# Optimization experiments

Hardware: AMD Instinct MI355X
Metric: run time of the kernel (lower is better)

Reference implementation:

```python
import jax, jax.numpy as jnp
import numpy as np

DIM = 256
HEADS = 8
HEAD_DIM = DIM // HEADS
WS = (2, 8, 8)  # window size (t, h, w)
N = WS[0] * WS[1] * WS[2]  # 128 tokens per window
SCALE = HEAD_DIM ** -0.5
MLP_HIDDEN = int(DIM * 2.0)
EPS = 1e-5

# static relative-position index table [N, N]
def _rel_pos_index():
    coords = np.stack(np.meshgrid(np.arange(WS[0]), np.arange(WS[1]), np.arange(WS[2]), indexing='ij'))
    cf = coords.reshape(3, -1)
    rel = cf[:, :, None] - cf[:, None, :]
    rel = rel.transpose(1, 2, 0).copy()
    rel[..., 0] += WS[0] - 1
    rel[..., 1] += WS[1] - 1
    rel[..., 2] += WS[2] - 1
    rel[..., 0] *= (2 * WS[1] - 1) * (2 * WS[2] - 1)
    rel[..., 1] *= (2 * WS[2] - 1)
    return rel.sum(-1)

REL_IDX = jnp.asarray(_rel_pos_index())  # [N, N] int
TABLE_SIZE = (2 * WS[0] - 1) * (2 * WS[1] - 1) * (2 * WS[2] - 1)  # 675


def layernorm(x, g, b):
    m = jnp.mean(x, axis=-1, keepdims=True)
    var = jnp.mean(jnp.square(x - m), axis=-1, keepdims=True)
    return (x - m) * jax.lax.rsqrt(var + EPS) * g + b


def window_partition(x):
    B, T, H, W, C = x.shape
    x = x.reshape(B, T // WS[0], WS[0], H // WS[1], WS[1], W // WS[2], WS[2], C)
    x = x.transpose(0, 1, 3, 5, 2, 4, 6, 7)
    return x.reshape(-1, N, C)


def window_reverse(wins, B, T, H, W):
    C = wins.shape[-1]
    x = wins.reshape(B, T // WS[0], H // WS[1], W // WS[2], WS[0], WS[1], WS[2], C)
    x = x.transpose(0, 1, 4, 2, 5, 3, 6, 7)
    return x.reshape(B, T, H, W, C)


def setup_inputs() -> dict:
    key = jax.random.key(0)
    ks = jax.random.split(key, 20)
    B, T, H, W = 2, 8, 64, 64
    f = lambda k, s, sc=0.02: jax.random.normal(k, s, dtype=jnp.float32) * sc
    return {
        'q': jax.random.normal(ks[0], (B, T, H, W, DIM), dtype=jnp.float32),
        'k': jax.random.normal(ks[1], (B, T, H, W, DIM), dtype=jnp.float32),
        'v': jax.random.normal(ks[2], (B, T, H, W, DIM), dtype=jnp.float32),
        'gq': jnp.ones((DIM,), jnp.float32), 'bq': jnp.zeros((DIM,), jnp.float32),
        'gk': jnp.ones((DIM,), jnp.float32), 'bk': jnp.zeros((DIM,), jnp.float32),
        'gv': jnp.ones((DIM,), jnp.float32), 'bv': jnp.zeros((DIM,), jnp.float32),
        'bias_table': f(ks[3], (TABLE_SIZE, HEADS)),
        'proj_w': f(ks[4], (DIM, DIM)), 'proj_b': jnp.zeros((DIM,), jnp.float32),
        'g2': jnp.ones((DIM,), jnp.float32), 'b2': jnp.zeros((DIM,), jnp.float32),
        'mw1': f(ks[5], (MLP_HIDDEN, DIM)), 'mb1': jnp.zeros((MLP_HIDDEN,), jnp.float32),
        'mw2': f(ks[6], (DIM, MLP_HIDDEN)), 'mb2': jnp.zeros((DIM,), jnp.float32),
    }


def reference(q, k, v, gq, bq, gk, bk, gv, bv, bias_table, proj_w, proj_b, g2, b2, mw1, mb1, mw2, mb2):
    B, T, H, W, C = q.shape
    shortcut = v
    qn = layernorm(q, gq, bq)
    kn = layernorm(k, gk, bk)
    vn = layernorm(v, gv, bv)
    # (dims divisible by window -> no padding needed)
    qw = window_partition(qn)  # [B_, N, C]
    kw = window_partition(kn)
    vw = window_partition(vn)
    B_ = qw.shape[0]
    to_heads = lambda t: t.reshape(B_, N, HEADS, HEAD_DIM).transpose(0, 2, 1, 3)  # [B_, h, N, d]
    qh, kh, vh = to_heads(qw), to_heads(kw), to_heads(vw)
    attn = jnp.einsum('bhnd,bhmd->bhnm', qh * SCALE, kh)
    bias = bias_table[REL_IDX]  # [N, N, heads]
    attn = attn + bias.transpose(2, 0, 1)[None]
    attn = jax.nn.softmax(attn, axis=-1)
    out = jnp.einsum('bhnm,bhmd->bhnd', attn, vh)
    out = out.transpose(0, 2, 1, 3).reshape(B_, N, C)
    out = out @ proj_w.T + proj_b
    x = window_reverse(out, B, T, H, W)
    x = shortcut + x
    h1 = layernorm(x, g2, b2)
    h1 = jax.nn.gelu(h1 @ mw1.T + mb1, approximate=False)
    x = x + (h1 @ mw2.T + mb2)
    return x
```

## Files before the change

kernel.cpp:

```cpp
#include <hip/hip_runtime.h>
#include <math.h>


typedef __attribute__((ext_vector_type(8))) short short8;
typedef __attribute__((ext_vector_type(4))) short shortx4;
typedef __attribute__((ext_vector_type(4))) float floatx4;

#define MFMA16(a, b, c) __builtin_amdgcn_mfma_f32_16x16x32_bf16((a), (b), (c), 0, 0, 0)
#define ATT_SCALE 0.17677669529663689f

__device__ __forceinline__ short f2bf(float f) {
  unsigned u = __float_as_uint(f);
  u += 0x7fffu + ((u >> 16) & 1u);
  return (short)(u >> 16);
}
__device__ __forceinline__ float bf2f(short s) {
  return __uint_as_float(((unsigned)(unsigned short)s) << 16);
}
__device__ __forceinline__ void gl2lds(const short* g, short* l) {
  __builtin_amdgcn_global_load_lds((const __attribute__((address_space(1))) void*)(g),
                                   (__attribute__((address_space(3))) void*)(l), 16, 0, 0);
}

__global__ void cvt_kernel(const float* __restrict__ src, short* __restrict__ dst, int n) {
  int i = blockIdx.x * 256 + threadIdx.x;
  if (i < n) dst[i] = f2bf(src[i]);
}

__global__ void biasprep_kernel(const float* __restrict__ table, short* __restrict__ biasPb) {
  int idx = blockIdx.x * 256 + threadIdx.x;
  int h = idx >> 14;
  int n = (idx >> 7) & 127;
  int lr = (idx >> 3) & 15;
  int c = idx & 7;
  int m = 16 * c + lr;
  int t1 = n >> 6, h1 = (n >> 3) & 7, w1 = n & 7;
  int t2 = m >> 6, h2 = (m >> 3) & 7, w2 = m & 7;
  int ridx = (t1 - t2 + 1) * 225 + (h1 - h2 + 7) * 15 + (w1 - w2 + 7);
  biasPb[idx] = f2bf(table[ridx * 8 + h]);
}

__global__ __launch_bounds__(256) void ln_qkv_kernel(
    const float* __restrict__ q, const float* __restrict__ k, const float* __restrict__ v,
    const float* __restrict__ gq, const float* __restrict__ bq,
    const float* __restrict__ gk, const float* __restrict__ bk,
    const float* __restrict__ gv, const float* __restrict__ bv,
    short* __restrict__ qw, short* __restrict__ kw, short* __restrict__ vw) {
  const int wv = threadIdx.x >> 6, l = threadIdx.x & 63;
  const int tok = blockIdx.x * 4 + wv;
  const int which = blockIdx.y;
  const float* src = (which == 0) ? q : ((which == 1) ? k : v);
  const float* gg  = (which == 0) ? gq : ((which == 1) ? gk : gv);
  const float* bb  = (which == 0) ? bq : ((which == 1) ? bk : bv);
  short* dst       = (which == 0) ? qw : ((which == 1) ? kw : vw);

  float4 xv = *(const float4*)(src + (size_t)tok * 256 + l * 4);
  float s1 = xv.x + xv.y + xv.z + xv.w;
  float s2 = xv.x * xv.x + xv.y * xv.y + xv.z * xv.z + xv.w * xv.w;
#pragma unroll
  for (int off = 1; off < 64; off <<= 1) {
    s1 += __shfl_xor(s1, off);
    s2 += __shfl_xor(s2, off);
  }
  float mean = s1 * (1.0f / 256.0f);
  float var = s2 * (1.0f / 256.0f) - mean * mean;
  float inv = rsqrtf(var + 1e-5f);

  int b_ = tok >> 15, rem = tok & 32767;
  int t = rem >> 12, hh = (rem >> 6) & 63, ww = rem & 63;
  int wi = ((b_ * 4 + (t >> 1)) * 8 + (hh >> 3)) * 8 + (ww >> 3);
  int n = ((t & 1) << 6) | ((hh & 7) << 3) | (ww & 7);

  float4 g4 = *(const float4*)(gg + l * 4);
  float4 b4 = *(const float4*)(bb + l * 4);
  shortx4 o;
  o[0] = f2bf((xv.x - mean) * inv * g4.x + b4.x);
  o[1] = f2bf((xv.y - mean) * inv * g4.y + b4.y);
  o[2] = f2bf((xv.z - mean) * inv * g4.z + b4.z);
  o[3] = f2bf((xv.w - mean) * inv * g4.w + b4.w);
  *(shortx4*)(dst + ((size_t)wi * 128 + n) * 256 + l * 4) = o;
}

__global__ __launch_bounds__(256, 4) void attn_kernel(
    const short* __restrict__ qw, const short* __restrict__ kw, const short* __restrict__ vw,
    const short* __restrict__ biasPb, short* __restrict__ ao) {
  __shared__ union SU {
    struct { short Qs[128][40]; short Ks[128][40]; } qk;
    short Ps[128 * 128];
  } su;
  __shared__ short Vt[32 * 128];

  const int wi = blockIdx.x, h = blockIdx.y, tid = threadIdx.x;
  const size_t base = (size_t)wi * 128 * 256 + h * 32;

#pragma unroll
  for (int i = 0; i < 2; ++i) {
    int idx = tid + 256 * i;
    int m = idx >> 2, c = idx & 3;
    *(short8*)&su.qk.Qs[m][c * 8] = *(const short8*)(qw + base + (size_t)m * 256 + c * 8);
    *(short8*)&su.qk.Ks[m][c * 8] = *(const short8*)(kw + base + (size_t)m * 256 + c * 8);
    short8 vv = *(const short8*)(vw + base + (size_t)m * 256 + c * 8);
#pragma unroll
    for (int e = 0; e < 8; ++e) {
      int d = c * 8 + e;
      Vt[d * 128 + (((m >> 3) ^ (d & 7)) << 3) + (m & 7)] = vv[e];
    }
  }
  __syncthreads();

  const int wvv = tid >> 6, l = tid & 63, lr = l & 15, g = l >> 4;
  const floatx4 zf = {0.f, 0.f, 0.f, 0.f};

  short8 aq0 = *(const short8*)&su.qk.Qs[32 * wvv + lr][g * 8];
  short8 aq1 = *(const short8*)&su.qk.Qs[32 * wvv + 16 + lr][g * 8];

  floatx4 s[2][8];
#pragma unroll
  for (int c = 0; c < 8; ++c) {
    short8 bk8 = *(const short8*)&su.qk.Ks[16 * c + lr][g * 8];
    s[0][c] = MFMA16(aq0, bk8, zf);
    s[1][c] = MFMA16(aq1, bk8, zf);
  }
  __syncthreads();

  const int lr7 = lr & 7;
#pragma unroll
  for (int r = 0; r < 2; ++r) {
#pragma unroll
    for (int j = 0; j < 4; ++j) {
      int n = 32 * wvv + 16 * r + 4 * g + j;
      short8 bv8 = *(const short8*)(biasPb + ((size_t)(h * 128 + n) * 16 + lr) * 8);
      float mx = -1e30f;
#pragma unroll
      for (int c = 0; c < 8; ++c) {
        float val = s[r][c][j] * ATT_SCALE + bf2f(bv8[c]);
        s[r][c][j] = val;
        mx = fmaxf(mx, val);
      }
#pragma unroll
      for (int off = 1; off < 16; off <<= 1) mx = fmaxf(mx, __shfl_xor(mx, off));
      float sum = 0.f;
#pragma unroll
      for (int c = 0; c < 8; ++c) {
        float e = __expf(s[r][c][j] - mx);
        s[r][c][j] = e;
        sum += e;
      }
#pragma unroll
      for (int off = 1; off < 16; off <<= 1) sum += __shfl_xor(sum, off);
      float invs = 1.0f / sum;
      int n7 = n & 7;
#pragma unroll
      for (int c = 0; c < 8; ++c) {
        int col = 16 * c + lr;
        su.Ps[n * 128 + (((col >> 3) ^ n7) << 3) + (col & 7)] = f2bf(s[r][c][j] * invs);
      }
    }
  }

  floatx4 o00 = zf, o01 = zf, o10 = zf, o11 = zf;
  const int ra0 = 32 * wvv + lr, ra1 = ra0 + 16;
#pragma unroll
  for (int ks = 0; ks < 4; ++ks) {
    int ulog = ks * 4 + g;
    short8 pa0 = *(const short8*)&su.Ps[ra0 * 128 + ((ulog ^ (ra0 & 7)) << 3)];
    short8 pa1 = *(const short8*)&su.Ps[ra1 * 128 + ((ulog ^ (ra1 & 7)) << 3)];
    short8 vb0 = *(const short8*)&Vt[lr * 128 + ((ulog ^ lr7) << 3)];
    short8 vb1 = *(const short8*)&Vt[(16 + lr) * 128 + ((ulog ^ lr7) << 3)];
    o00 = MFMA16(pa0, vb0, o00);
    o01 = MFMA16(pa0, vb1, o01);
    o10 = MFMA16(pa1, vb0, o10);
    o11 = MFMA16(pa1, vb1, o11);
  }
#pragma unroll
  for (int j = 0; j < 4; ++j) {
    int n0 = 32 * wvv + 4 * g + j;
    int n1 = n0 + 16;
    size_t rb0 = ((size_t)wi * 128 + n0) * 256 + h * 32;
    size_t rb1 = ((size_t)wi * 128 + n1) * 256 + h * 32;
    ao[rb0 + lr] = f2bf(o00[j]);
    ao[rb0 + 16 + lr] = f2bf(o01[j]);
    ao[rb1 + lr] = f2bf(o10[j]);
    ao[rb1 + 16 + lr] = f2bf(o11[j]);
  }
}

__global__ __launch_bounds__(512, 1) void xpath_kernel(
    const short* __restrict__ ao, const short* __restrict__ wp,
    const float* __restrict__ proj_b, const float* __restrict__ vin,
    const float* __restrict__ g2, const float* __restrict__ b2,
    const short* __restrict__ w1, const float* __restrict__ mb1,
    const short* __restrict__ w2, const float* __restrict__ mb2,
    float* __restrict__ out) {
  __shared__ short Ws[256 * 64];
  __shared__ short XL[128 * 256];
  __shared__ short H1[128 * 128];

  const int tid = threadIdx.x;
  const int w = tid >> 6, l = tid & 63, lr = l & 15, g = l >> 4;
  const int li = l >> 3, u = l & 7;
  const int swz = ((u ^ li) << 3);
  const int s0 = ((g ^ (lr & 7)) << 3);
  const int s1 = (((4 + g) ^ (lr & 7)) << 3);
  const floatx4 zf = {0.f, 0.f, 0.f, 0.f};
  const int bx = blockIdx.x;
  const int r16 = 16 * w + lr;
  const size_t grow = (size_t)bx * 128;

  floatx4 acc1[16];
#pragma unroll
  for (int i = 0; i < 16; ++i) acc1[i] = zf;
  for (int k0 = 0; k0 < 256; k0 += 64) {
    short8 a0 = *(const short8*)(ao + (grow + r16) * 256 + k0 + g * 8);
    short8 a1 = *(const short8*)(ao + (grow + r16) * 256 + k0 + 32 + g * 8);
    __syncthreads();
#pragma unroll
    for (int i = 0; i < 4; ++i) {
      int c = w + 8 * i;
      gl2lds(wp + (size_t)(8 * c + li) * 256 + k0 + swz, Ws + c * 512);
    }
    __syncthreads();
#pragma unroll
    for (int ct = 0; ct < 16; ++ct) {
      int rb = ct * 16 + lr;
      short8 b0 = *(const short8*)&Ws[rb * 64 + s0];
      acc1[ct] = MFMA16(a0, b0, acc1[ct]);
      short8 b1 = *(const short8*)&Ws[rb * 64 + s1];
      acc1[ct] = MFMA16(a1, b1, acc1[ct]);
    }
  }

  int sidx4[4];
  float xr[16][4];
  {
    const int wb = bx & 7, hb = (bx >> 3) & 7, tt = (bx >> 6) & 3, b_ = bx >> 8;
#pragma unroll
    for (int j = 0; j < 4; ++j) {
      int row = 16 * w + 4 * g + j;
      int t = tt * 2 + (row >> 6), hh = hb * 8 + ((row >> 3) & 7), ww2 = wb * 8 + (row & 7);
      int sidx = ((b_ * 8 + t) * 64 + hh) * 64 + ww2;
      sidx4[j] = sidx;
      float ss1 = 0.f, ss2 = 0.f;
#pragma unroll
      for (int ct = 0; ct < 16; ++ct) {
        int col = ct * 16 + lr;
        float val = acc1[ct][j] + proj_b[col] + vin[(size_t)sidx * 256 + col];
        xr[ct][j] = val;
        ss1 += val;
        ss2 += val * val;
      }
#pragma unroll
      for (int off = 1; off < 16; off <<= 1) {
        ss1 += __shfl_xor(ss1, off);
        ss2 += __shfl_xor(ss2, off);
      }
      float mean = ss1 * (1.0f / 256.0f);
      float var = ss2 * (1.0f / 256.0f) - mean * mean;
      float inv = rsqrtf(var + 1e-5f);
      int r7 = row & 7;
#pragma unroll
      for (int ct = 0; ct < 16; ++ct) {
        int col = ct * 16 + lr;
        float xl = (xr[ct][j] - mean) * inv * g2[col] + b2[col];
        int uu = col >> 3;
        XL[row * 256 + (((uu & 24) | ((uu & 7) ^ r7)) << 3) + (col & 7)] = f2bf(xl);
      }
    }
  }

  floatx4 acc3[16];
#pragma unroll
  for (int i = 0; i < 16; ++i) acc3[i] = zf;

  for (int qt = 0; qt < 4; ++qt) {
    floatx4 acc2[8];
#pragma unroll
    for (int i = 0; i < 8; ++i) acc2[i] = zf;
    for (int k0 = 0; k0 < 256; k0 += 64) {
      __syncthreads();
#pragma unroll
      for (int i = 0; i < 2; ++i) {
        int c = w + 8 * i;
        gl2lds(w1 + (size_t)(qt * 128 + 8 * c + li) * 256 + k0 + swz, Ws + c * 512);
      }
      __syncthreads();
      short8 a0 = *(const short8*)&XL[r16 * 256 + k0 + ((g ^ (r16 & 7)) << 3)];
      short8 a1 = *(const short8*)&XL[r16 * 256 + k0 + (((4 + g) ^ (r16 & 7)) << 3)];
#pragma unroll
      for (int ct = 0; ct < 8; ++ct) {
        int rb = ct * 16 + lr;
        short8 b0 = *(const short8*)&Ws[rb * 64 + s0];
        acc2[ct] = MFMA16(a0, b0, acc2[ct]);
        short8 b1 = *(const short8*)&Ws[rb * 64 + s1];
        acc2[ct] = MFMA16(a1, b1, acc2[ct]);
      }
    }
#pragma unroll
    for (int ct = 0; ct < 8; ++ct) {
      int col = ct * 16 + lr;
      float bias = mb1[qt * 128 + col];
#pragma unroll
      for (int j = 0; j < 4; ++j) {
        int row = 16 * w + 4 * g + j;
        float val = acc2[ct][j] + bias;
        float ge = 0.5f * val * (1.0f + erff(val * 0.70710678118654752f));
        int uu = col >> 3;
        H1[row * 128 + (((uu & 8) | ((uu & 7) ^ (row & 7))) << 3) + (col & 7)] = f2bf(ge);
      }
    }
    for (int k0 = 0; k0 < 128; k0 += 64) {
      __syncthreads();
#pragma unroll
      for (int i = 0; i < 4; ++i) {
        int c = w + 8 * i;
        gl2lds(w2 + (size_t)(8 * c + li) * 512 + qt * 128 + k0 + swz, Ws + c * 512);
      }
      __syncthreads();
      short8 a0 = *(const short8*)&H1[r16 * 128 + k0 + ((g ^ (r16 & 7)) << 3)];
      short8 a1 = *(const short8*)&H1[r16 * 128 + k0 + (((4 + g) ^ (r16 & 7)) << 3)];
#pragma unroll
      for (int ct = 0; ct < 16; ++ct) {
        int rb = ct * 16 + lr;
        short8 b0 = *(const short8*)&Ws[rb * 64 + s0];
        acc3[ct] = MFMA16(a0, b0, acc3[ct]);
        short8 b1 = *(const short8*)&Ws[rb * 64 + s1];
        acc3[ct] = MFMA16(a1, b1, acc3[ct]);
      }
    }
  }

#pragma unroll
  for (int ct = 0; ct < 16; ++ct) {
    int col = ct * 16 + lr;
    float bias = mb2[col];
#pragma unroll
    for (int j = 0; j < 4; ++j)
      out[(size_t)sidx4[j] * 256 + col] = xr[ct][j] + acc3[ct][j] + bias;
  }
}

extern "C" void kernel_launch(void* const* d_in, const int* in_sizes, int n_in,
                              void* d_out, int out_size, void* d_ws, size_t ws_size,
                              hipStream_t stream) {
  const float* q = (const float*)d_in[0];
  const float* k = (const float*)d_in[1];
  const float* v = (const float*)d_in[2];
  const float* gq = (const float*)d_in[3];
  const float* bq = (const float*)d_in[4];
  const float* gk = (const float*)d_in[5];
  const float* bk = (const float*)d_in[6];
  const float* gv = (const float*)d_in[7];
  const float* bv = (const float*)d_in[8];
  const float* bias_table = (const float*)d_in[9];
  const float* proj_w = (const float*)d_in[10];
  const float* proj_b = (const float*)d_in[11];
  const float* g2 = (const float*)d_in[12];
  const float* b2 = (const float*)d_in[13];
  const float* mw1 = (const float*)d_in[14];
  const float* mb1 = (const float*)d_in[15];
  const float* mw2 = (const float*)d_in[16];
  const float* mb2 = (const float*)d_in[17];

  char* ws = (char*)d_ws;
  short* qw = (short*)(ws + 0);
  short* kw = (short*)(ws + 33554432);
  short* vw = (short*)(ws + 67108864);
  short* ao = (short*)(ws + 100663296);
  short* wp = (short*)(ws + 167772160);
  short* w1 = (short*)(ws + 167903232);
  short* w2 = (short*)(ws + 168165376);
  short* biasPb = (short*)(ws + 168427520);

  cvt_kernel<<<256, 256, 0, stream>>>(proj_w, wp, 65536);
  cvt_kernel<<<512, 256, 0, stream>>>(mw1, w1, 131072);
  cvt_kernel<<<512, 256, 0, stream>>>(mw2, w2, 131072);
  biasprep_kernel<<<512, 256, 0, stream>>>(bias_table, biasPb);

  ln_qkv_kernel<<<dim3(16384, 3), 256, 0, stream>>>(q, k, v, gq, bq, gk, bk, gv, bv, qw, kw, vw);

  attn_kernel<<<dim3(512, 8), 256, 0, stream>>>(qw, kw, vw, biasPb, ao);

  xpath_kernel<<<512, 512, 0, stream>>>(ao, wp, proj_b, v, g2, b2, w1, mb1, w2, mb2,
                                        (float*)d_out);
}
```

Before: 225.8 us.

## Double-buffer weight tiles in fused projection/MLP kernel to overlap loads with MFMA

Splits the shared weight staging buffer into two LDS buffers and restructures the projection, fc1 and fc2 loops into an unrolled ping-pong pipeline. Each stage issues the next weight tile's global-to-LDS load before running the MFMAs on the current tile, and fc2's last stage prefetches the next quarter's fc1 tile. A single waitcnt-plus-barrier replaces the two __syncthreads per step. This aims to hide global load latency and cut barrier count, at the cost of doubling weight LDS to a large total footprint that leaves no slack.

```diff
diff --git a/kernel.cpp b/kernel.cpp
--- a/kernel.cpp
+++ b/kernel.cpp
@@ -8,6 +8,13 @@
 
 #define MFMA16(a, b, c) __builtin_amdgcn_mfma_f32_16x16x32_bf16((a), (b), (c), 0, 0, 0)
 #define ATT_SCALE 0.17677669529663689f
+
+#define PIPE_SYNC()                                  \
+  do {                                               \
+    asm volatile("s_waitcnt vmcnt(0)" ::: "memory"); \
+    __builtin_amdgcn_s_barrier();                    \
+    __builtin_amdgcn_sched_barrier(0);               \
+  } while (0)
 
 __device__ __forceinline__ short f2bf(float f) {
   unsigned u = __float_as_uint(f);
@@ -192,7 +199,8 @@
     const short* __restrict__ w1, const float* __restrict__ mb1,
     const short* __restrict__ w2, const float* __restrict__ mb2,
     float* __restrict__ out) {
-  __shared__ short Ws[256 * 64];
+  __shared__ short Ws0[256 * 64];
+  __shared__ short Ws1[256 * 64];
   __shared__ short XL[128 * 256];
   __shared__ short H1[128 * 128];
 
@@ -207,28 +215,70 @@
   const int r16 = 16 * w + lr;
   const size_t grow = (size_t)bx * 128;
 
-  floatx4 acc1[16];
-#pragma unroll
-  for (int i = 0; i < 16; ++i) acc1[i] = zf;
-  for (int k0 = 0; k0 < 256; k0 += 64) {
-    short8 a0 = *(const short8*)(ao + (grow + r16) * 256 + k0 + g * 8);
-    short8 a1 = *(const short8*)(ao + (grow + r16) * 256 + k0 + 32 + g * 8);
-    __syncthreads();
+  auto stP = [&](short* dst, int k0) {
 #pragma unroll
     for (int i = 0; i < 4; ++i) {
       int c = w + 8 * i;
-      gl2lds(wp + (size_t)(8 * c + li) * 256 + k0 + swz, Ws + c * 512);
-    }
-    __syncthreads();
+      gl2lds(wp + (size_t)(8 * c + li) * 256 + k0 + swz, dst + c * 512);
+    }
+  };
+  auto st1 = [&](short* dst, int qt, int k0) {
+#pragma unroll
+    for (int i = 0; i < 2; ++i) {
+      int c = w + 8 * i;
+      gl2lds(w1 + (size_t)(qt * 128 + 8 * c + li) * 256 + k0 + swz, dst + c * 512);
+    }
+  };
+  auto st2 = [&](short* dst, int qt, int k0) {
+#pragma unroll
+    for (int i = 0; i < 4; ++i) {
+      int c = w + 8 * i;
+      gl2lds(w2 + (size_t)(8 * c + li) * 512 + qt * 128 + k0 + swz, dst + c * 512);
+    }
+  };
+  auto mm16 = [&](const short* Wb, short8 a0, short8 a1, floatx4* acc) {
 #pragma unroll
     for (int ct = 0; ct < 16; ++ct) {
       int rb = ct * 16 + lr;
-      short8 b0 = *(const short8*)&Ws[rb * 64 + s0];
-      acc1[ct] = MFMA16(a0, b0, acc1[ct]);
-      short8 b1 = *(const short8*)&Ws[rb * 64 + s1];
-      acc1[ct] = MFMA16(a1, b1, acc1[ct]);
-    }
-  }
+      acc[ct] = MFMA16(a0, *(const short8*)&Wb[rb * 64 + s0], acc[ct]);
+      acc[ct] = MFMA16(a1, *(const short8*)&Wb[rb * 64 + s1], acc[ct]);
+    }
+  };
+  auto mm8 = [&](const short* Wb, short8 a0, short8 a1, floatx4* acc) {
+#pragma unroll
+    for (int ct = 0; ct < 8; ++ct) {
+      int rb = ct * 16 + lr;
+      acc[ct] = MFMA16(a0, *(const short8*)&Wb[rb * 64 + s0], acc[ct]);
+      acc[ct] = MFMA16(a1, *(const short8*)&Wb[rb * 64 + s1], acc[ct]);
+    }
+  };
+
+  short8 pa[8];
+#pragma unroll
+  for (int t = 0; t < 4; ++t) {
+    pa[2 * t] = *(const short8*)(ao + (grow + r16) * 256 + 64 * t + g * 8);
+    pa[2 * t + 1] = *(const short8*)(ao + (grow + r16) * 256 + 64 * t + 32 + g * 8);
+  }
+
+  floatx4 acc1[16];
+#pragma unroll
+  for (int i = 0; i < 16; ++i) acc1[i] = zf;
+
+  stP(Ws0, 0);
+  PIPE_SYNC();
+
+  stP(Ws1, 64);
+  mm16(Ws0, pa[0], pa[1], acc1);
+  PIPE_SYNC();
+  stP(Ws0, 128);
+  mm16(Ws1, pa[2], pa[3], acc1);
+  PIPE_SYNC();
+  stP(Ws1, 192);
+  mm16(Ws0, pa[4], pa[5], acc1);
+  PIPE_SYNC();
+  st1(Ws0, 0, 0);
+  mm16(Ws1, pa[6], pa[7], acc1);
+  PIPE_SYNC();
 
   int sidx4[4];
   float xr[16][4];
@@ -276,25 +326,26 @@
     floatx4 acc2[8];
 #pragma unroll
     for (int i = 0; i < 8; ++i) acc2[i] = zf;
-    for (int k0 = 0; k0 < 256; k0 += 64) {
-      __syncthreads();
-#pragma unroll
-      for (int i = 0; i < 2; ++i) {
-        int c = w + 8 * i;
-        gl2lds(w1 + (size_t)(qt * 128 + 8 * c + li) * 256 + k0 + swz, Ws + c * 512);
-      }
-      __syncthreads();
-      short8 a0 = *(const short8*)&XL[r16 * 256 + k0 + ((g ^ (r16 & 7)) << 3)];
-      short8 a1 = *(const short8*)&XL[r16 * 256 + k0 + (((4 + g) ^ (r16 & 7)) << 3)];
-#pragma unroll
-      for (int ct = 0; ct < 8; ++ct) {
-        int rb = ct * 16 + lr;
-        short8 b0 = *(const short8*)&Ws[rb * 64 + s0];
-        acc2[ct] = MFMA16(a0, b0, acc2[ct]);
-        short8 b1 = *(const short8*)&Ws[rb * 64 + s1];
-        acc2[ct] = MFMA16(a1, b1, acc2[ct]);
-      }
-    }
+    const int xb = r16 * 256, x7 = r16 & 7;
+    const int h1b = r16 * 128;
+
+    st1(Ws1, qt, 64);
+    mm8(Ws0, *(const short8*)&XL[xb + 0 + ((g ^ x7) << 3)],
+        *(const short8*)&XL[xb + 0 + (((4 + g) ^ x7) << 3)], acc2);
+    PIPE_SYNC();
+    st1(Ws0, qt, 128);
+    mm8(Ws1, *(const short8*)&XL[xb + 64 + ((g ^ x7) << 3)],
+        *(const short8*)&XL[xb + 64 + (((4 + g) ^ x7) << 3)], acc2);
+    PIPE_SYNC();
+    st1(Ws1, qt, 192);
+    mm8(Ws0, *(const short8*)&XL[xb + 128 + ((g ^ x7) << 3)],
+        *(const short8*)&XL[xb + 128 + (((4 + g) ^ x7) << 3)], acc2);
+    PIPE_SYNC();
+    st2(Ws0, qt, 0);
+    mm8(Ws1, *(const short8*)&XL[xb + 192 + ((g ^ x7) << 3)],
+        *(const short8*)&XL[xb + 192 + (((4 + g) ^ x7) << 3)], acc2);
+    PIPE_SYNC();
+
 #pragma unroll
     for (int ct = 0; ct < 8; ++ct) {
       int col = ct * 16 + lr;
@@ -308,25 +359,15 @@
         H1[row * 128 + (((uu & 8) | ((uu & 7) ^ (row & 7))) << 3) + (col & 7)] = f2bf(ge);
       }
     }
-    for (int k0 = 0; k0 < 128; k0 += 64) {
-      __syncthreads();
-#pragma unroll
-      for (int i = 0; i < 4; ++i) {
-        int c = w + 8 * i;
-        gl2lds(w2 + (size_t)(8 * c + li) * 512 + qt * 128 + k0 + swz, Ws + c * 512);
-      }
-      __syncthreads();
-      short8 a0 = *(const short8*)&H1[r16 * 128 + k0 + ((g ^ (r16 & 7)) << 3)];
-      short8 a1 = *(const short8*)&H1[r16 * 128 + k0 + (((4 + g) ^ (r16 & 7)) << 3)];
-#pragma unroll
-      for (int ct = 0; ct < 16; ++ct) {
-        int rb = ct * 16 + lr;
-        short8 b0 = *(const short8*)&Ws[rb * 64 + s0];
-        acc3[ct] = MFMA16(a0, b0, acc3[ct]);
-        short8 b1 = *(const short8*)&Ws[rb * 64 + s1];
-        acc3[ct] = MFMA16(a1, b1, acc3[ct]);
-      }
-    }
+
+    st2(Ws1, qt, 64);
+    mm16(Ws0, *(const short8*)&H1[h1b + 0 + ((g ^ x7) << 3)],
+         *(const short8*)&H1[h1b + 0 + (((4 + g) ^ x7) << 3)], acc3);
+    PIPE_SYNC();
+    if (qt < 3) st1(Ws0, qt + 1, 0);
+    mm16(Ws1, *(const short8*)&H1[h1b + 64 + ((g ^ x7) << 3)],
+         *(const short8*)&H1[h1b + 64 + (((4 + g) ^ x7) << 3)], acc3);
+    PIPE_SYNC();
   }
 
 #pragma unroll
```

Result: no change. 229.6 us (+1.7%).

## Pipeline MLP kernel weights through triple-buffered LDS with 2D wave tiling

Applied to the files above, without the earlier changes.

Rewrites the fused projection, LayerNorm and MLP kernel. Weight tiles for proj, W1 and W2 now stream through a three-slot LDS ring, using explicit vmcnt waits and single barriers, so loads overlap the MFMA work. Work is split across waves on a 2x4 (row by column) grid, which needs a small shared-memory reduction for the LayerNorm statistics. It also swaps the exact erf GELU for a tanh-style sigmoid approximation, which adds a small numerical deviation from the reference.

```diff
diff --git a/kernel.cpp b/kernel.cpp
--- a/kernel.cpp
+++ b/kernel.cpp
@@ -8,6 +8,15 @@
 
 #define MFMA16(a, b, c) __builtin_amdgcn_mfma_f32_16x16x32_bf16((a), (b), (c), 0, 0, 0)
 #define ATT_SCALE 0.17677669529663689f
+
+#define WAITV2() asm volatile("s_waitcnt vmcnt(2)" ::: "memory")
+#define WAITV0() asm volatile("s_waitcnt vmcnt(0)" ::: "memory")
+#define LGKM0() asm volatile("s_waitcnt lgkmcnt(0)" ::: "memory")
+#define BARSYNC()                       \
+  do {                                  \
+    __builtin_amdgcn_s_barrier();       \
+    __builtin_amdgcn_sched_barrier(0);  \
+  } while (0)
 
 __device__ __forceinline__ short f2bf(float f) {
   unsigned u = __float_as_uint(f);
@@ -185,158 +194,256 @@
   }
 }
 
-__global__ __launch_bounds__(512, 1) void xpath_kernel(
+__global__ __launch_bounds__(512, 2) void xpath_kernel(
     const short* __restrict__ ao, const short* __restrict__ wp,
     const float* __restrict__ proj_b, const float* __restrict__ vin,
     const float* __restrict__ g2, const float* __restrict__ b2,
     const short* __restrict__ w1, const float* __restrict__ mb1,
     const short* __restrict__ w2, const float* __restrict__ mb2,
     float* __restrict__ out) {
-  __shared__ short Ws[256 * 64];
+  __shared__ short BUF[3 * 8192];
   __shared__ short XL[128 * 256];
   __shared__ short H1[128 * 128];
+  __shared__ float2 RED[128][4];
 
   const int tid = threadIdx.x;
   const int w = tid >> 6, l = tid & 63, lr = l & 15, g = l >> 4;
-  const int li = l >> 3, u = l & 7;
-  const int swz = ((u ^ li) << 3);
-  const int s0 = ((g ^ (lr & 7)) << 3);
-  const int s1 = (((4 + g) ^ (lr & 7)) << 3);
+  const int wm = w >> 2, wn = w & 3;
   const floatx4 zf = {0.f, 0.f, 0.f, 0.f};
   const int bx = blockIdx.x;
-  const int r16 = 16 * w + lr;
-  const size_t grow = (size_t)bx * 128;
-
-  floatx4 acc1[16];
-#pragma unroll
-  for (int i = 0; i < 16; ++i) acc1[i] = zf;
-  for (int k0 = 0; k0 < 256; k0 += 64) {
-    short8 a0 = *(const short8*)(ao + (grow + r16) * 256 + k0 + g * 8);
-    short8 a1 = *(const short8*)(ao + (grow + r16) * 256 + k0 + 32 + g * 8);
-    __syncthreads();
-#pragma unroll
-    for (int i = 0; i < 4; ++i) {
-      int c = w + 8 * i;
-      gl2lds(wp + (size_t)(8 * c + li) * 256 + k0 + swz, Ws + c * 512);
-    }
-    __syncthreads();
-#pragma unroll
-    for (int ct = 0; ct < 16; ++ct) {
-      int rb = ct * 16 + lr;
-      short8 b0 = *(const short8*)&Ws[rb * 64 + s0];
-      acc1[ct] = MFMA16(a0, b0, acc1[ct]);
-      short8 b1 = *(const short8*)&Ws[rb * 64 + s1];
-      acc1[ct] = MFMA16(a1, b1, acc1[ct]);
-    }
-  }
-
-  int sidx4[4];
-  float xr[16][4];
+  const int wb = bx & 7, hb = (bx >> 3) & 7, tt2 = (bx >> 6) & 3, b_ = bx >> 8;
+
+  const int p0 = (w * 2) * 64 + l, p1 = p0 + 64;
+  const int rA0 = ((p0 >> 5) << 3) | (p0 & 7), uA0 = (p0 >> 3) & 3;
+  const int rA1 = ((p1 >> 5) << 3) | (p1 & 7), uA1 = (p1 >> 3) & 3;
+  const int rB0 = ((p0 >> 6) << 3) | (p0 & 7), uB0 = (p0 >> 3) & 7;
+  const int rB1 = ((p1 >> 6) << 3) | (p1 & 7), uB1 = (p1 >> 3) & 7;
+
+  int ra[4], ra7[4];
+#pragma unroll
+  for (int mt = 0; mt < 4; ++mt) {
+    ra[mt] = wm * 64 + mt * 16 + lr;
+    ra7[mt] = ra[mt] & 7;
+  }
+  int cF[4], cQ[2];
+#pragma unroll
+  for (int nt = 0; nt < 4; ++nt) {
+    int rb = wn * 64 + nt * 16 + lr;
+    cF[nt] = ((rb >> 3) << 8) | ((rb & 7) << 3);
+  }
+#pragma unroll
+  for (int nt = 0; nt < 2; ++nt) {
+    int rb = wn * 32 + nt * 16 + lr;
+    cQ[nt] = ((rb >> 3) << 9) | ((rb & 7) << 3);
+  }
+
+  auto stage_wp = [&](short* dst, int k0) {
+    gl2lds(wp + (size_t)rA0 * 256 + k0 + uA0 * 8, dst + (w * 2) * 512);
+    gl2lds(wp + (size_t)rA1 * 256 + k0 + uA1 * 8, dst + (w * 2 + 1) * 512);
+  };
+  auto stage_w1 = [&](short* dst, int qt, int k0) {
+    gl2lds(w1 + (size_t)(qt * 128 + rB0) * 256 + k0 + uB0 * 8, dst + (w * 2) * 512);
+    gl2lds(w1 + (size_t)(qt * 128 + rB1) * 256 + k0 + uB1 * 8, dst + (w * 2 + 1) * 512);
+  };
+  auto stage_w2 = [&](short* dst, int k) {
+    gl2lds(w2 + (size_t)rA0 * 512 + k + uA0 * 8, dst + (w * 2) * 512);
+    gl2lds(w2 + (size_t)rA1 * 512 + k + uA1 * 8, dst + (w * 2 + 1) * 512);
+  };
+
+  const short* aoB = ao + (size_t)bx * 128 * 256;
+
+  floatx4 acc1[4][4];
+#pragma unroll
+  for (int mt = 0; mt < 4; ++mt)
+#pragma unroll
+    for (int nt = 0; nt < 4; ++nt) acc1[mt][nt] = zf;
+
+  stage_wp(BUF, 0);
+  stage_wp(BUF + 8192, 32);
+  short8 a[2][4];
+#pragma unroll
+  for (int mt = 0; mt < 4; ++mt)
+    a[0][mt] = *(const short8*)(aoB + (size_t)ra[mt] * 256 + g * 8);
+
+#pragma unroll
+  for (int s = 0; s < 8; ++s) {
+    WAITV2();
+    BARSYNC();
+    if (s < 6) stage_wp(BUF + ((s + 2) % 3) * 8192, 32 * (s + 2));
+    else if (s == 6) stage_w1(BUF + 2 * 8192, 0, 0);
+    else stage_w1(BUF, 0, 64);
+    if (s < 7) {
+#pragma unroll
+      for (int mt = 0; mt < 4; ++mt)
+        a[(s + 1) & 1][mt] =
+            *(const short8*)(aoB + (size_t)ra[mt] * 256 + 32 * (s + 1) + g * 8);
+    }
+    const short* bb = BUF + (s % 3) * 8192;
+    short8 b[4];
+#pragma unroll
+    for (int nt = 0; nt < 4; ++nt) b[nt] = *(const short8*)&bb[cF[nt] + (g << 6)];
+#pragma unroll
+    for (int mt = 0; mt < 4; ++mt)
+#pragma unroll
+      for (int nt = 0; nt < 4; ++nt)
+        acc1[mt][nt] = MFMA16(a[s & 1][mt], b[nt], acc1[mt][nt]);
+  }
+
   {
-    const int wb = bx & 7, hb = (bx >> 3) & 7, tt = (bx >> 6) & 3, b_ = bx >> 8;
+    float pbv[4], g2v[4], b2v[4];
+#pragma unroll
+    for (int nt = 0; nt < 4; ++nt) {
+      int col = wn * 64 + nt * 16 + lr;
+      pbv[nt] = proj_b[col];
+      g2v[nt] = g2[col];
+      b2v[nt] = b2[col];
+    }
+#pragma unroll
+    for (int mt = 0; mt < 4; ++mt) {
+#pragma unroll
+      for (int j = 0; j < 4; ++j) {
+        int row = wm * 64 + mt * 16 + 4 * g + j;
+        int t = tt2 * 2 + (row >> 6), hh = hb * 8 + ((row >> 3) & 7), ww2 = wb * 8 + (row & 7);
+        size_t sidx = ((size_t)(b_ * 8 + t) * 64 + hh) * 64 + ww2;
+        float s1 = 0.f, s2 = 0.f;
+#pragma unroll
+        for (int nt = 0; nt < 4; ++nt) {
+          float val = acc1[mt][nt][j] + pbv[nt] + vin[sidx * 256 + wn * 64 + nt * 16 + lr];
+          acc1[mt][nt][j] = val;
+          s1 += val;
+          s2 += val * val;
+        }
+#pragma unroll
+        for (int off = 1; off < 16; off <<= 1) {
+          s1 += __shfl_xor(s1, off);
+          s2 += __shfl_xor(s2, off);
+        }
+        if (lr == 0) RED[row][wn] = make_float2(s1, s2);
+      }
+    }
+    LGKM0();
+    BARSYNC();
+#pragma unroll
+    for (int mt = 0; mt < 4; ++mt) {
+#pragma unroll
+      for (int j = 0; j < 4; ++j) {
+        int row = wm * 64 + mt * 16 + 4 * g + j;
+        float2 r0 = RED[row][0], r1 = RED[row][1], r2 = RED[row][2], r3 = RED[row][3];
+        float mean = (r0.x + r1.x + r2.x + r3.x) * (1.0f / 256.0f);
+        float var = (r0.y + r1.y + r2.y + r3.y) * (1.0f / 256.0f) - mean * mean;
+        float inv = rsqrtf(var + 1e-5f);
+        int r7 = row & 7;
+#pragma unroll
+        for (int nt = 0; nt < 4; ++nt) {
+          int col = wn * 64 + nt * 16 + lr;
+          float xlv = (acc1[mt][nt][j] - mean) * inv * g2v[nt] + b2v[nt];
+          int u = col >> 3;
+          XL[row * 256 + (((u & 24) | ((u & 7) ^ r7)) << 3) + (col & 7)] = f2bf(xlv);
+        }
+      }
+    }
+    LGKM0();
+  }
+
+  floatx4 acc3[4][4];
+#pragma unroll
+  for (int mt = 0; mt < 4; ++mt)
+#pragma unroll
+    for (int nt = 0; nt < 4; ++nt) acc3[mt][nt] = zf;
+
+#pragma unroll 1
+  for (int qt = 0; qt < 4; ++qt) {
+    floatx4 acc2[4][2];
+#pragma unroll
+    for (int mt = 0; mt < 4; ++mt)
+#pragma unroll
+      for (int nt = 0; nt < 2; ++nt) acc2[mt][nt] = zf;
+    float mb1v[2];
+
+#pragma unroll
+    for (int t = 0; t < 8; ++t) {
+      if (qt == 3 && t == 7) { WAITV0(); } else { WAITV2(); }
+      BARSYNC();
+      const int sb = (2 + 2 * qt + t) % 3;
+      const short* bb = BUF + sb * 8192;
+      short* sd = BUF + ((sb + 2) % 3) * 8192;
+      if (t < 2) stage_w1(sd, qt, 64 * (t + 2));
+      else if (t < 6) stage_w2(sd, qt * 128 + 32 * (t - 2));
+      else if (qt < 3) stage_w1(sd, qt + 1, 64 * (t - 6));
+      if (t == 0) {
+#pragma unroll
+        for (int nt = 0; nt < 2; ++nt) mb1v[nt] = mb1[qt * 128 + wn * 32 + nt * 16 + lr];
+      }
+
+      if (t < 4) {
+#pragma unroll
+        for (int ks = 0; ks < 2; ++ks) {
+          short8 xa[4], xb[2];
+#pragma unroll
+          for (int mt = 0; mt < 4; ++mt)
+            xa[mt] = *(const short8*)&XL[ra[mt] * 256 + 64 * t + (((4 * ks + g) ^ ra7[mt]) << 3)];
+#pragma unroll
+          for (int nt = 0; nt < 2; ++nt)
+            xb[nt] = *(const short8*)&bb[cQ[nt] + ((4 * ks + g) << 6)];
+#pragma unroll
+          for (int mt = 0; mt < 4; ++mt)
+#pragma unroll
+            for (int nt = 0; nt < 2; ++nt)
+              acc2[mt][nt] = MFMA16(xa[mt], xb[nt], acc2[mt][nt]);
+        }
+        if (t == 3) {
+#pragma unroll
+          for (int mt = 0; mt < 4; ++mt)
+#pragma unroll
+            for (int nt = 0; nt < 2; ++nt) {
+              int col = wn * 32 + nt * 16 + lr;
+              int u = col >> 3;
+#pragma unroll
+              for (int j = 0; j < 4; ++j) {
+                int row = wm * 64 + mt * 16 + 4 * g + j;
+                float xv = acc2[mt][nt][j] + mb1v[nt];
+                float yy = 1.5957691216057308f * (xv + 0.044715f * xv * xv * xv);
+                float sg = 1.0f / (1.0f + __expf(-yy));
+                H1[row * 128 + (((u & 8) | ((u & 7) ^ (row & 7))) << 3) + (col & 7)] =
+                    f2bf(xv * sg);
+              }
+            }
+          LGKM0();
+        }
+      } else {
+        const int u0 = 4 * (t - 4);
+        short8 ha[4], hbv[4];
+#pragma unroll
+        for (int mt = 0; mt < 4; ++mt) {
+          int u = u0 + g;
+          ha[mt] = *(const short8*)&H1[ra[mt] * 128 + (((u & 8) | ((u & 7) ^ ra7[mt])) << 3)];
+        }
+#pragma unroll
+        for (int nt = 0; nt < 4; ++nt) hbv[nt] = *(const short8*)&bb[cF[nt] + (g << 6)];
+#pragma unroll
+        for (int mt = 0; mt < 4; ++mt)
+#pragma unroll
+          for (int nt = 0; nt < 4; ++nt)
+            acc3[mt][nt] = MFMA16(ha[mt], hbv[nt], acc3[mt][nt]);
+      }
+    }
+  }
+
+  float mb2v[4];
+#pragma unroll
+  for (int nt = 0; nt < 4; ++nt) mb2v[nt] = mb2[wn * 64 + nt * 16 + lr];
+#pragma unroll
+  for (int mt = 0; mt < 4; ++mt)
 #pragma unroll
     for (int j = 0; j < 4; ++j) {
-      int row = 16 * w + 4 * g + j;
-      int t = tt * 2 + (row >> 6), hh = hb * 8 + ((row >> 3) & 7), ww2 = wb * 8 + (row & 7);
-      int sidx = ((b_ * 8 + t) * 64 + hh) * 64 + ww2;
-      sidx4[j] = sidx;
-      float ss1 = 0.f, ss2 = 0.f;
-#pragma unroll
-      for (int ct = 0; ct < 16; ++ct) {
-        int col = ct * 16 + lr;
-        float val = acc1[ct][j] + proj_b[col] + vin[(size_t)sidx * 256 + col];
-        xr[ct][j] = val;
-        ss1 += val;
-        ss2 += val * val;
-      }
-#pragma unroll
-      for (int off = 1; off < 16; off <<= 1) {
-        ss1 += __shfl_xor(ss1, off);
-        ss2 += __shfl_xor(ss2, off);
-      }
-      float mean = ss1 * (1.0f / 256.0f);
-      float var = ss2 * (1.0f / 256.0f) - mean * mean;
-      float inv = rsqrtf(var + 1e-5f);
-      int r7 = row & 7;
-#pragma unroll
-      for (int ct = 0; ct < 16; ++ct) {
-        int col = ct * 16 + lr;
-        float xl = (xr[ct][j] - mean) * inv * g2[col] + b2[col];
-        int uu = col >> 3;
-        XL[row * 256 + (((uu & 24) | ((uu & 7) ^ r7)) << 3) + (col & 7)] = f2bf(xl);
-      }
-    }
-  }
-
-  floatx4 acc3[16];
-#pragma unroll
-  for (int i = 0; i < 16; ++i) acc3[i] = zf;
-
-  for (int qt = 0; qt < 4; ++qt) {
-    floatx4 acc2[8];
-#pragma unroll
-    for (int i = 0; i < 8; ++i) acc2[i] = zf;
-    for (int k0 = 0; k0 < 256; k0 += 64) {
-      __syncthreads();
-#pragma unroll
-      for (int i = 0; i < 2; ++i) {
-        int c = w + 8 * i;
-        gl2lds(w1 + (size_t)(qt * 128 + 8 * c + li) * 256 + k0 + swz, Ws + c * 512);
-      }
-      __syncthreads();
-      short8 a0 = *(const short8*)&XL[r16 * 256 + k0 + ((g ^ (r16 & 7)) << 3)];
-      short8 a1 = *(const short8*)&XL[r16 * 256 + k0 + (((4 + g) ^ (r16 & 7)) << 3)];
-#pragma unroll
-      for (int ct = 0; ct < 8; ++ct) {
-        int rb = ct * 16 + lr;
-        short8 b0 = *(const short8*)&Ws[rb * 64 + s0];
-        acc2[ct] = MFMA16(a0, b0, acc2[ct]);
-        short8 b1 = *(const short8*)&Ws[rb * 64 + s1];
-        acc2[ct] = MFMA16(a1, b1, acc2[ct]);
-      }
-    }
-#pragma unroll
-    for (int ct = 0; ct < 8; ++ct) {
-      int col = ct * 16 + lr;
-      float bias = mb1[qt * 128 + col];
-#pragma unroll
-      for (int j = 0; j < 4; ++j) {
-        int row = 16 * w + 4 * g + j;
-        float val = acc2[ct][j] + bias;
-        float ge = 0.5f * val * (1.0f + erff(val * 0.70710678118654752f));
-        int uu = col >> 3;
-        H1[row * 128 + (((uu & 8) | ((uu & 7) ^ (row & 7))) << 3) + (col & 7)] = f2bf(ge);
-      }
-    }
-    for (int k0 = 0; k0 < 128; k0 += 64) {
-      __syncthreads();
-#pragma unroll
-      for (int i = 0; i < 4; ++i) {
-        int c = w + 8 * i;
-        gl2lds(w2 + (size_t)(8 * c + li) * 512 + qt * 128 + k0 + swz, Ws + c * 512);
-      }
-      __syncthreads();
-      short8 a0 = *(const short8*)&H1[r16 * 128 + k0 + ((g ^ (r16 & 7)) << 3)];
-      short8 a1 = *(const short8*)&H1[r16 * 128 + k0 + (((4 + g) ^ (r16 & 7)) << 3)];
-#pragma unroll
-      for (int ct = 0; ct < 16; ++ct) {
-        int rb = ct * 16 + lr;
-        short8 b0 = *(const short8*)&Ws[rb * 64 + s0];
-        acc3[ct] = MFMA16(a0, b0, acc3[ct]);
-        short8 b1 = *(const short8*)&Ws[rb * 64 + s1];
-        acc3[ct] = MFMA16(a1, b1, acc3[ct]);
-      }
-    }
-  }
-
-#pragma unroll
-  for (int ct = 0; ct < 16; ++ct) {
-    int col = ct * 16 + lr;
-    float bias = mb2[col];
-#pragma unroll
-    for (int j = 0; j < 4; ++j)
-      out[(size_t)sidx4[j] * 256 + col] = xr[ct][j] + acc3[ct][j] + bias;
-  }
+      int row = wm * 64 + mt * 16 + 4 * g + j;
+      int t = tt2 * 2 + (row >> 6), hh = hb * 8 + ((row >> 3) & 7), ww2 = wb * 8 + (row & 7);
+      size_t sidx = ((size_t)(b_ * 8 + t) * 64 + hh) * 64 + ww2;
+#pragma unroll
+      for (int nt = 0; nt < 4; ++nt)
+        out[sidx * 256 + wn * 64 + nt * 16 + lr] =
+            acc1[mt][nt][j] + acc3[mt][nt][j] + mb2v[nt];
+    }
 }
 
 extern "C" void kernel_launch(void* const* d_in, const int* in_sizes, int n_in,
```

New measurement: 264.2 us. +17.0%, slower.

## Split fused proj/MLP kernel into three GEMM kernels with full weights in LDS

Applied to the files above, without the earlier changes.

Replaces the single fused projection+LayerNorm+MLP kernel with three kernels: proj+residual+LN, MLP1+GELU and MLP2+residual. Each keeps an entire weight slice resident in shared memory and processes 256 rows per block, with the MLP split across two column halves. This removes the repeated per-k-chunk weight staging and barriers of the fused kernel. The cost is round-tripping x, LN(x) and the hidden activations through global memory in bf16. It also swaps the exact erf GELU for a tanh/sigmoid approximation and stores the residual in bf16, which lowers accuracy.

```diff
diff --git a/kernel.cpp b/kernel.cpp
--- a/kernel.cpp
+++ b/kernel.cpp
@@ -16,10 +16,6 @@
 }
 __device__ __forceinline__ float bf2f(short s) {
   return __uint_as_float(((unsigned)(unsigned short)s) << 16);
-}
-__device__ __forceinline__ void gl2lds(const short* g, short* l) {
-  __builtin_amdgcn_global_load_lds((const __attribute__((address_space(1))) void*)(g),
-                                   (__attribute__((address_space(3))) void*)(l), 16, 0, 0);
 }
 
 __global__ void cvt_kernel(const float* __restrict__ src, short* __restrict__ dst, int n) {
@@ -185,157 +181,229 @@
   }
 }
 
-__global__ __launch_bounds__(512, 1) void xpath_kernel(
+__global__ __launch_bounds__(512, 2) void projln_kernel(
     const short* __restrict__ ao, const short* __restrict__ wp,
     const float* __restrict__ proj_b, const float* __restrict__ vin,
     const float* __restrict__ g2, const float* __restrict__ b2,
-    const short* __restrict__ w1, const float* __restrict__ mb1,
-    const short* __restrict__ w2, const float* __restrict__ mb2,
-    float* __restrict__ out) {
-  __shared__ short Ws[256 * 64];
-  __shared__ short XL[128 * 256];
-  __shared__ short H1[128 * 128];
+    short* __restrict__ xbf, short* __restrict__ xln) {
+  __shared__ short WS[256 * 256];
 
   const int tid = threadIdx.x;
   const int w = tid >> 6, l = tid & 63, lr = l & 15, g = l >> 4;
-  const int li = l >> 3, u = l & 7;
-  const int swz = ((u ^ li) << 3);
-  const int s0 = ((g ^ (lr & 7)) << 3);
-  const int s1 = (((4 + g) ^ (lr & 7)) << 3);
   const floatx4 zf = {0.f, 0.f, 0.f, 0.f};
-  const int bx = blockIdx.x;
-  const int r16 = 16 * w + lr;
-  const size_t grow = (size_t)bx * 128;
-
-  floatx4 acc1[16];
-#pragma unroll
-  for (int i = 0; i < 16; ++i) acc1[i] = zf;
-  for (int k0 = 0; k0 < 256; k0 += 64) {
-    short8 a0 = *(const short8*)(ao + (grow + r16) * 256 + k0 + g * 8);
-    short8 a1 = *(const short8*)(ao + (grow + r16) * 256 + k0 + 32 + g * 8);
-    __syncthreads();
-#pragma unroll
-    for (int i = 0; i < 4; ++i) {
-      int c = w + 8 * i;
-      gl2lds(wp + (size_t)(8 * c + li) * 256 + k0 + swz, Ws + c * 512);
-    }
-    __syncthreads();
+
+#pragma unroll
+  for (int c = 0; c < 16; ++c) {
+    int idx = tid * 16 + c;
+    int r = idx >> 5, u = idx & 31;
+    short8 vv = *(const short8*)(wp + (size_t)r * 256 + u * 8);
+    *(short8*)&WS[r * 256 + ((u ^ (r & 7)) << 3)] = vv;
+  }
+
+  const int rowbase = blockIdx.x * 256 + w * 32;
+  short8 a[2][8];
+#pragma unroll
+  for (int mt = 0; mt < 2; ++mt)
+#pragma unroll
+    for (int s = 0; s < 8; ++s)
+      a[mt][s] = *(const short8*)(ao + (size_t)(rowbase + mt * 16 + lr) * 256 + s * 32 + g * 8);
+
+  __syncthreads();
+
+  floatx4 acc[2][16];
+#pragma unroll
+  for (int mt = 0; mt < 2; ++mt)
+#pragma unroll
+    for (int ct = 0; ct < 16; ++ct) acc[mt][ct] = zf;
+
+#pragma unroll
+  for (int s = 0; s < 8; ++s) {
 #pragma unroll
     for (int ct = 0; ct < 16; ++ct) {
       int rb = ct * 16 + lr;
-      short8 b0 = *(const short8*)&Ws[rb * 64 + s0];
-      acc1[ct] = MFMA16(a0, b0, acc1[ct]);
-      short8 b1 = *(const short8*)&Ws[rb * 64 + s1];
-      acc1[ct] = MFMA16(a1, b1, acc1[ct]);
-    }
-  }
-
-  int sidx4[4];
-  float xr[16][4];
-  {
-    const int wb = bx & 7, hb = (bx >> 3) & 7, tt = (bx >> 6) & 3, b_ = bx >> 8;
+      short8 b = *(const short8*)&WS[rb * 256 + (((s * 4 + g) ^ (rb & 7)) << 3)];
+      acc[0][ct] = MFMA16(a[0][s], b, acc[0][ct]);
+      acc[1][ct] = MFMA16(a[1][s], b, acc[1][ct]);
+    }
+  }
+
+  float pb[16], g2v[16], b2v[16];
+#pragma unroll
+  for (int ct = 0; ct < 16; ++ct) {
+    int col = ct * 16 + lr;
+    pb[ct] = proj_b[col];
+    g2v[ct] = g2[col];
+    b2v[ct] = b2[col];
+  }
+#pragma unroll
+  for (int mt = 0; mt < 2; ++mt) {
 #pragma unroll
     for (int j = 0; j < 4; ++j) {
-      int row = 16 * w + 4 * g + j;
-      int t = tt * 2 + (row >> 6), hh = hb * 8 + ((row >> 3) & 7), ww2 = wb * 8 + (row & 7);
-      int sidx = ((b_ * 8 + t) * 64 + hh) * 64 + ww2;
-      sidx4[j] = sidx;
-      float ss1 = 0.f, ss2 = 0.f;
+      int wrow = rowbase + mt * 16 + 4 * g + j;
+      int wi = wrow >> 7, n = wrow & 127;
+      int wb = wi & 7, hb = (wi >> 3) & 7, tt = (wi >> 6) & 3, b_ = wi >> 8;
+      int t = tt * 2 + (n >> 6), hh = hb * 8 + ((n >> 3) & 7), ww2 = wb * 8 + (n & 7);
+      size_t sidx = ((size_t)(b_ * 8 + t) * 64 + hh) * 64 + ww2;
+      float xv[16], s1 = 0.f, s2 = 0.f;
+#pragma unroll
+      for (int ct = 0; ct < 16; ++ct) {
+        float val = acc[mt][ct][j] + pb[ct] + vin[sidx * 256 + ct * 16 + lr];
+        xv[ct] = val;
+        s1 += val;
+        s2 += val * val;
+      }
+#pragma unroll
+      for (int off = 1; off < 16; off <<= 1) {
+        s1 += __shfl_xor(s1, off);
+        s2 += __shfl_xor(s2, off);
+      }
+      float mean = s1 * (1.0f / 256.0f);
+      float var = s2 * (1.0f / 256.0f) - mean * mean;
+      float inv = rsqrtf(var + 1e-5f);
 #pragma unroll
       for (int ct = 0; ct < 16; ++ct) {
         int col = ct * 16 + lr;
-        float val = acc1[ct][j] + proj_b[col] + vin[(size_t)sidx * 256 + col];
-        xr[ct][j] = val;
-        ss1 += val;
-        ss2 += val * val;
-      }
-#pragma unroll
-      for (int off = 1; off < 16; off <<= 1) {
-        ss1 += __shfl_xor(ss1, off);
-        ss2 += __shfl_xor(ss2, off);
-      }
-      float mean = ss1 * (1.0f / 256.0f);
-      float var = ss2 * (1.0f / 256.0f) - mean * mean;
-      float inv = rsqrtf(var + 1e-5f);
-      int r7 = row & 7;
+        xbf[(size_t)wrow * 256 + col] = f2bf(xv[ct]);
+        xln[(size_t)wrow * 256 + col] = f2bf((xv[ct] - mean) * inv * g2v[ct] + b2v[ct]);
+      }
+    }
+  }
+}
+
+__global__ __launch_bounds__(512, 2) void mlp1_kernel(
+    const short* __restrict__ xln, const short* __restrict__ w1,
+    const float* __restrict__ mb1, short* __restrict__ h1) {
+  __shared__ short WS[256 * 256];
+
+  const int tid = threadIdx.x;
+  const int w = tid >> 6, l = tid & 63, lr = l & 15, g = l >> 4;
+  const int half = blockIdx.y;
+  const floatx4 zf = {0.f, 0.f, 0.f, 0.f};
+  const short* w1h = w1 + (size_t)half * 256 * 256;
+
+#pragma unroll
+  for (int c = 0; c < 16; ++c) {
+    int idx = tid * 16 + c;
+    int r = idx >> 5, u = idx & 31;
+    short8 vv = *(const short8*)(w1h + (size_t)r * 256 + u * 8);
+    *(short8*)&WS[r * 256 + ((u ^ (r & 7)) << 3)] = vv;
+  }
+
+  const int rowbase = blockIdx.x * 256 + w * 32;
+  short8 a[2][8];
+#pragma unroll
+  for (int mt = 0; mt < 2; ++mt)
+#pragma unroll
+    for (int s = 0; s < 8; ++s)
+      a[mt][s] = *(const short8*)(xln + (size_t)(rowbase + mt * 16 + lr) * 256 + s * 32 + g * 8);
+
+  __syncthreads();
+
+  floatx4 acc[2][16];
+#pragma unroll
+  for (int mt = 0; mt < 2; ++mt)
+#pragma unroll
+    for (int ct = 0; ct < 16; ++ct) acc[mt][ct] = zf;
+
+#pragma unroll
+  for (int s = 0; s < 8; ++s) {
+#pragma unroll
+    for (int ct = 0; ct < 16; ++ct) {
+      int rb = ct * 16 + lr;
+      short8 b = *(const short8*)&WS[rb * 256 + (((s * 4 + g) ^ (rb & 7)) << 3)];
+      acc[0][ct] = MFMA16(a[0][s], b, acc[0][ct]);
+      acc[1][ct] = MFMA16(a[1][s], b, acc[1][ct]);
+    }
+  }
+
+  float bias[16];
+#pragma unroll
+  for (int ct = 0; ct < 16; ++ct) bias[ct] = mb1[half * 256 + ct * 16 + lr];
+#pragma unroll
+  for (int mt = 0; mt < 2; ++mt) {
+#pragma unroll
+    for (int j = 0; j < 4; ++j) {
+      int wrow = rowbase + mt * 16 + 4 * g + j;
 #pragma unroll
       for (int ct = 0; ct < 16; ++ct) {
-        int col = ct * 16 + lr;
-        float xl = (xr[ct][j] - mean) * inv * g2[col] + b2[col];
-        int uu = col >> 3;
-        XL[row * 256 + (((uu & 24) | ((uu & 7) ^ r7)) << 3) + (col & 7)] = f2bf(xl);
-      }
-    }
-  }
-
-  floatx4 acc3[16];
-#pragma unroll
-  for (int i = 0; i < 16; ++i) acc3[i] = zf;
-
-  for (int qt = 0; qt < 4; ++qt) {
-    floatx4 acc2[8];
-#pragma unroll
-    for (int i = 0; i < 8; ++i) acc2[i] = zf;
-    for (int k0 = 0; k0 < 256; k0 += 64) {
-      __syncthreads();
-#pragma unroll
-      for (int i = 0; i < 2; ++i) {
-        int c = w + 8 * i;
-        gl2lds(w1 + (size_t)(qt * 128 + 8 * c + li) * 256 + k0 + swz, Ws + c * 512);
-      }
-      __syncthreads();
-      short8 a0 = *(const short8*)&XL[r16 * 256 + k0 + ((g ^ (r16 & 7)) << 3)];
-      short8 a1 = *(const short8*)&XL[r16 * 256 + k0 + (((4 + g) ^ (r16 & 7)) << 3)];
+        float xv = acc[mt][ct][j] + bias[ct];
+        float yy = 1.5957691216057308f * (xv + 0.044715f * xv * xv * xv);
+        float sg = 1.0f / (1.0f + __expf(-yy));
+        h1[(size_t)wrow * 512 + half * 256 + ct * 16 + lr] = f2bf(xv * sg);
+      }
+    }
+  }
+}
+
+__global__ __launch_bounds__(512, 2) void mlp2_kernel(
+    const short* __restrict__ h1, const short* __restrict__ w2,
+    const float* __restrict__ mb2, const short* __restrict__ xbf,
+    float* __restrict__ out) {
+  __shared__ short WS[128 * 512];
+
+  const int tid = threadIdx.x;
+  const int w = tid >> 6, l = tid & 63, lr = l & 15, g = l >> 4;
+  const int half = blockIdx.y;
+  const floatx4 zf = {0.f, 0.f, 0.f, 0.f};
+  const short* w2h = w2 + (size_t)half * 128 * 512;
+
+#pragma unroll
+  for (int c = 0; c < 16; ++c) {
+    int idx = tid * 16 + c;
+    int r = idx >> 6, u = idx & 63;
+    short8 vv = *(const short8*)(w2h + (size_t)r * 512 + u * 8);
+    *(short8*)&WS[r * 512 + ((u ^ (r & 7)) << 3)] = vv;
+  }
+  __syncthreads();
+
+  const int rowbase = blockIdx.x * 256 + w * 32;
+  floatx4 acc[2][8];
+#pragma unroll
+  for (int mt = 0; mt < 2; ++mt)
+#pragma unroll
+    for (int ct = 0; ct < 8; ++ct) acc[mt][ct] = zf;
+
+#pragma unroll
+  for (int hk = 0; hk < 2; ++hk) {
+    short8 a[2][8];
+#pragma unroll
+    for (int mt = 0; mt < 2; ++mt)
+#pragma unroll
+      for (int s = 0; s < 8; ++s)
+        a[mt][s] = *(const short8*)(h1 + (size_t)(rowbase + mt * 16 + lr) * 512 +
+                                    hk * 256 + s * 32 + g * 8);
+#pragma unroll
+    for (int s = 0; s < 8; ++s) {
+      int S = hk * 8 + s;
 #pragma unroll
       for (int ct = 0; ct < 8; ++ct) {
         int rb = ct * 16 + lr;
-        short8 b0 = *(const short8*)&Ws[rb * 64 + s0];
-        acc2[ct] = MFMA16(a0, b0, acc2[ct]);
-        short8 b1 = *(const short8*)&Ws[rb * 64 + s1];
-        acc2[ct] = MFMA16(a1, b1, acc2[ct]);
-      }
-    }
-#pragma unroll
-    for (int ct = 0; ct < 8; ++ct) {
-      int col = ct * 16 + lr;
-      float bias = mb1[qt * 128 + col];
-#pragma unroll
-      for (int j = 0; j < 4; ++j) {
-        int row = 16 * w + 4 * g + j;
-        float val = acc2[ct][j] + bias;
-        float ge = 0.5f * val * (1.0f + erff(val * 0.70710678118654752f));
-        int uu = col >> 3;
-        H1[row * 128 + (((uu & 8) | ((uu & 7) ^ (row & 7))) << 3) + (col & 7)] = f2bf(ge);
-      }
-    }
-    for (int k0 = 0; k0 < 128; k0 += 64) {
-      __syncthreads();
-#pragma unroll
-      for (int i = 0; i < 4; ++i) {
-        int c = w + 8 * i;
-        gl2lds(w2 + (size_t)(8 * c + li) * 512 + qt * 128 + k0 + swz, Ws + c * 512);
-      }
-      __syncthreads();
-      short8 a0 = *(const short8*)&H1[r16 * 128 + k0 + ((g ^ (r16 & 7)) << 3)];
-      short8 a1 = *(const short8*)&H1[r16 * 128 + k0 + (((4 + g) ^ (r16 & 7)) << 3)];
-#pragma unroll
-      for (int ct = 0; ct < 16; ++ct) {
-        int rb = ct * 16 + lr;
-        short8 b0 = *(const short8*)&Ws[rb * 64 + s0];
-        acc3[ct] = MFMA16(a0, b0, acc3[ct]);
-        short8 b1 = *(const short8*)&Ws[rb * 64 + s1];
-        acc3[ct] = MFMA16(a1, b1, acc3[ct]);
-      }
-    }
-  }
-
-#pragma unroll
-  for (int ct = 0; ct < 16; ++ct) {
-    int col = ct * 16 + lr;
-    float bias = mb2[col];
-#pragma unroll
-    for (int j = 0; j < 4; ++j)
-      out[(size_t)sidx4[j] * 256 + col] = xr[ct][j] + acc3[ct][j] + bias;
+        short8 b = *(const short8*)&WS[rb * 512 + (((S * 4 + g) ^ (rb & 7)) << 3)];
+        acc[0][ct] = MFMA16(a[0][s], b, acc[0][ct]);
+        acc[1][ct] = MFMA16(a[1][s], b, acc[1][ct]);
+      }
+    }
+  }
+
+  float bias[8];
+#pragma unroll
+  for (int ct = 0; ct < 8; ++ct) bias[ct] = mb2[half * 128 + ct * 16 + lr];
+#pragma unroll
+  for (int mt = 0; mt < 2; ++mt) {
+#pragma unroll
+    for (int j = 0; j < 4; ++j) {
+      int wrow = rowbase + mt * 16 + 4 * g + j;
+      int wi = wrow >> 7, n = wrow & 127;
+      int wb = wi & 7, hb = (wi >> 3) & 7, tt = (wi >> 6) & 3, b_ = wi >> 8;
+      int t = tt * 2 + (n >> 6), hh = hb * 8 + ((n >> 3) & 7), ww2 = wb * 8 + (n & 7);
+      size_t sidx = ((size_t)(b_ * 8 + t) * 64 + hh) * 64 + ww2;
+#pragma unroll
+      for (int ct = 0; ct < 8; ++ct) {
+        int col = half * 128 + ct * 16 + lr;
+        out[sidx * 256 + col] =
+            bf2f(xbf[(size_t)wrow * 256 + col]) + acc[mt][ct][j] + bias[ct];
+      }
+    }
   }
 }
 
@@ -366,6 +434,9 @@
   short* kw = (short*)(ws + 33554432);
   short* vw = (short*)(ws + 67108864);
   short* ao = (short*)(ws + 100663296);
+  short* xln = (short*)(ws + 0);
+  short* xbf = (short*)(ws + 33554432);
+  short* h1 = (short*)(ws + 67108864);
   short* wp = (short*)(ws + 167772160);
   short* w1 = (short*)(ws + 167903232);
   short* w2 = (short*)(ws + 168165376);
@@ -380,6 +451,9 @@
 
   attn_kernel<<<dim3(512, 8), 256, 0, stream>>>(qw, kw, vw, biasPb, ao);
 
-  xpath_kernel<<<512, 512, 0, stream>>>(ao, wp, proj_b, v, g2, b2, w1, mb1, w2, mb2,
-                                        (float*)d_out);
-}
+  projln_kernel<<<256, 512, 0, stream>>>(ao, wp, proj_b, v, g2, b2, xbf, xln);
+
+  mlp1_kernel<<<dim3(256, 2), 512, 0, stream>>>(xln, w1, mb1, h1);
+
+  mlp2_kernel<<<dim3(256, 2), 512, 0, stream>>>(h1, w2, mb2, xbf, (float*)d_out);
+}
```

Result: slower. 256.5 us (+13.6%).
